# Kernel optimization log

Measured on AMD Instinct MI355X. Metric: run time of the kernel, lower is better.

Reference implementation:

```python
import jax, jax.numpy as jnp
import numpy as np

N_NODES = 50000
N_EDGES = 500000
IN_DIM = 64
OUT_DIM = 64
NUM_RELS = 16


def setup_inputs() -> dict:
    key = jax.random.key(0)
    ks = jax.random.split(key, 8)
    h = jax.random.normal(ks[0], (N_NODES, IN_DIM), dtype=jnp.float32)
    he = jax.random.normal(ks[1], (N_EDGES, IN_DIM), dtype=jnp.float32)
    src = jax.random.randint(ks[2], (N_EDGES,), 0, N_NODES)
    dst = jax.random.randint(ks[3], (N_EDGES,), 0, N_NODES)
    rel = jax.random.randint(ks[4], (N_EDGES,), 0, NUM_RELS)
    # xavier-ish scales
    W_shared = jax.random.normal(ks[5], (OUT_DIM, IN_DIM), dtype=jnp.float32) * (2.0 / (IN_DIM + OUT_DIM)) ** 0.5
    W_attn = jax.random.normal(ks[6], (1, 3 * OUT_DIM), dtype=jnp.float32) * (2.0 / (3 * OUT_DIM + 1)) ** 0.5
    W_rel = jax.random.normal(ks[7], (NUM_RELS, IN_DIM, OUT_DIM), dtype=jnp.float32) * (2.0 / (IN_DIM + OUT_DIM)) ** 0.5
    return {"h": h, "he": he, "src": src, "dst": dst, "rel": rel,
            "W_shared": W_shared, "W_attn": W_attn, "W_rel": W_rel}


def reference(h, he, src, dst, rel, W_shared, W_attn, W_rel):
    # --- edge attention: a = attn_fc([z_src, z_edge, z_dst]) (raw linear score, no softmax in original) ---
    Z = h @ W_shared.T                      # [N, out] project all nodes once
    ze = he @ W_shared.T                    # [E, out]
    # split attn weight to avoid materializing [E, 3*out] concat
    Wa_s, Wa_e, Wa_d = jnp.split(W_attn, 3, axis=1)   # each [1, out]
    a = Z[src] @ Wa_s.T + ze @ Wa_e.T + Z[dst] @ Wa_d.T   # [E, 1]
    # --- message: msg = (h_src @ W_rel[rel]) * a ---
    # compute per-(node, relation) transform once [N, R, out], then gather per edge
    H_all = jnp.einsum('ni,rio->nro', h, W_rel)          # [N, R, out]
    msg = H_all[src, rel] * a                             # [E, out]
    # --- scatter-sum aggregation into destination nodes ---
    out = jax.ops.segment_sum(msg, dst, num_segments=N_NODES)  # [N, out]
    # apply_func: activation (relu), no bias
    return jax.nn.relu(out)
```

## Files before the change

### kernel.cpp

```cpp
#include <hip/hip_runtime.h>
#include <math.h>

#define N_NODES 50000
#define N_EDGES 500000
#define DIM 64
#define NUM_RELS 16
#define GPB 64


__global__ void k0_prep(const float* __restrict__ W_shared,
                        const float* __restrict__ W_attn,
                        float* __restrict__ uvecs,
                        int* __restrict__ counts,
                        int* __restrict__ cursor) {
    int t = threadIdx.x;
    if (t < 64) {
        float us = 0.f, ve = 0.f, ud = 0.f;
        for (int o = 0; o < 64; ++o) {
            float w = W_shared[o * 64 + t];
            us = fmaf(w, W_attn[o],        us);
            ve = fmaf(w, W_attn[64 + o],   ve);
            ud = fmaf(w, W_attn[128 + o],  ud);
        }
        uvecs[t] = us; uvecs[64 + t] = ve; uvecs[128 + t] = ud;
    } else if (t < 80) {
        counts[t - 64] = 0;
    } else if (t < 96) {
        cursor[t - 80] = 0;
    }
}

__global__ void k1_node(const float* __restrict__ h,
                        const float* __restrict__ uvecs,
                        float* __restrict__ sn, float* __restrict__ dn,
                        float4* __restrict__ out4) {
    int n = blockIdx.x * blockDim.x + threadIdx.x;
    if (n >= N_NODES) return;
    const float* hp = h + (size_t)n * DIM;
    float s = 0.f, d = 0.f;
#pragma unroll
    for (int i = 0; i < 64; i += 4) {
        float4 t = *(const float4*)(hp + i);
        s = fmaf(t.x, uvecs[i],     s); s = fmaf(t.y, uvecs[i + 1], s);
        s = fmaf(t.z, uvecs[i + 2], s); s = fmaf(t.w, uvecs[i + 3], s);
        d = fmaf(t.x, uvecs[128 + i],     d); d = fmaf(t.y, uvecs[128 + i + 1], d);
        d = fmaf(t.z, uvecs[128 + i + 2], d); d = fmaf(t.w, uvecs[128 + i + 3], d);
    }
    sn[n] = s; dn[n] = d;
    float4 z = make_float4(0.f, 0.f, 0.f, 0.f);
#pragma unroll
    for (int i = 0; i < 16; ++i) out4[(size_t)n * 16 + i] = z;
}

__global__ void k2_ae(const float4* __restrict__ he4,
                      const int* __restrict__ src, const int* __restrict__ dst,
                      const int* __restrict__ rel,
                      const float* __restrict__ uvecs,
                      const float* __restrict__ sn, const float* __restrict__ dn,
                      float* __restrict__ ae, int* __restrict__ counts) {
    __shared__ int hist[NUM_RELS];
    int t = threadIdx.x;
    if (t < NUM_RELS) hist[t] = 0;
    __syncthreads();

    const int lane = t & 63;
    const int sub  = lane & 3;
    const int eo   = lane >> 2;
    const int gw   = blockIdx.x * 4 + (t >> 6);
    const int nw   = gridDim.x * 4;

    float4 u0 = *(const float4*)(uvecs + 64 + sub * 16 + 0);
    float4 u1 = *(const float4*)(uvecs + 64 + sub * 16 + 4);
    float4 u2 = *(const float4*)(uvecs + 64 + sub * 16 + 8);
    float4 u3 = *(const float4*)(uvecs + 64 + sub * 16 + 12);

    for (int base = gw * 16; base < N_EDGES; base += nw * 16) {
        int e = base + eo;
        float p = 0.f;
        if (e < N_EDGES) {
            const float4* row = he4 + (size_t)e * 16 + sub * 4;
            float4 a = row[0], b = row[1], c = row[2], d = row[3];
            p = a.x*u0.x + a.y*u0.y + a.z*u0.z + a.w*u0.w
              + b.x*u1.x + b.y*u1.y + b.z*u1.z + b.w*u1.w
              + c.x*u2.x + c.y*u2.y + c.z*u2.z + c.w*u2.w
              + d.x*u3.x + d.y*u3.y + d.z*u3.z + d.w*u3.w;
        }
        p += __shfl_xor(p, 1, 64);
        p += __shfl_xor(p, 2, 64);
        if (sub == 0 && e < N_EDGES) {
            ae[e] = p + sn[src[e]] + dn[dst[e]];
            atomicAdd(&hist[rel[e]], 1);
        }
    }
    __syncthreads();
    if (t < NUM_RELS && hist[t]) atomicAdd(&counts[t], hist[t]);
}

__global__ void k3_scan(const int* __restrict__ counts, int* __restrict__ offs) {
    int acc = 0;
    for (int r = 0; r < NUM_RELS; ++r) { offs[r] = acc; acc += counts[r]; }
    offs[NUM_RELS] = acc;
}

__global__ void k4_scatter(const int* __restrict__ rel,
                           const int* __restrict__ offs,
                           int* __restrict__ cursor,
                           int* __restrict__ perm) {
    __shared__ int hist[NUM_RELS];
    __shared__ int bbase[NUM_RELS];
    int t = threadIdx.x;
    if (t < NUM_RELS) hist[t] = 0;
    __syncthreads();
    int e = blockIdx.x * 1024 + t;
    int r = 0, lpos = 0;
    bool valid = (e < N_EDGES);
    if (valid) { r = rel[e]; lpos = atomicAdd(&hist[r], 1); }
    __syncthreads();
    if (t < NUM_RELS) bbase[t] = hist[t] ? atomicAdd(&cursor[t], hist[t]) : 0;
    __syncthreads();
    if (valid) perm[offs[r] + bbase[r] + lpos] = e;
}

__global__ __launch_bounds__(256, 4) void k5_main(
    const float* __restrict__ h,
    const int* __restrict__ src, const int* __restrict__ dst,
    const float* __restrict__ W_rel,
    const float* __restrict__ ae,
    const int* __restrict__ offs, const int* __restrict__ perm,
    float* __restrict__ out)
{
    const int lane = threadIdx.x & 63;
    const int wib  = __builtin_amdgcn_readfirstlane(threadIdx.x >> 6);
    const int r    = blockIdx.x & 15;
    const int g    = blockIdx.x >> 4;
    const int wr   = g * 4 + wib;
    const int WPR  = GPB * 4;

    float w[64];
    const float* wb = W_rel + (size_t)r * (DIM * DIM) + lane;
#pragma unroll
    for (int i = 0; i < 64; ++i) w[i] = wb[i * 64];
#pragma unroll
    for (int i = 0; i < 64; ++i) asm volatile("" : "+v"(w[i]));

    const int begin = offs[r];
    const int end   = offs[r + 1];

    for (int base = begin + wr * 64; base < end; base += WPR * 64) {
        int e_l = 0, s_l = 0, d_l = 0; float a_l = 0.f;
        if (base + lane < end) {
            e_l = perm[base + lane];
            s_l = src[e_l];
            d_l = dst[e_l];
            a_l = ae[e_l];
        }
        const int kmax = min(64, end - base);
        for (int k = 0; k < kmax; ++k) {
            const int   si = __builtin_amdgcn_readlane(s_l, k);
            const int   di = __builtin_amdgcn_readlane(d_l, k);
            const float ak = __int_as_float(__builtin_amdgcn_readlane(__float_as_int(a_l), k));

            const float* hp = h + (size_t)si * DIM;
            float a0 = 0.f, a1 = 0.f, a2 = 0.f, a3 = 0.f;
#pragma unroll
            for (int i = 0; i < 64; i += 4) {
                a0 = fmaf(hp[i],     w[i],     a0);
                a1 = fmaf(hp[i + 1], w[i + 1], a1);
                a2 = fmaf(hp[i + 2], w[i + 2], a2);
                a3 = fmaf(hp[i + 3], w[i + 3], a3);
            }
            const float dot = (a0 + a1) + (a2 + a3);
            unsafeAtomicAdd(out + (size_t)di * DIM + lane, ak * dot);
        }
    }
}

__global__ void k6_relu(float4* __restrict__ out, int n4) {
    int i = blockIdx.x * blockDim.x + threadIdx.x;
    if (i < n4) {
        float4 v = out[i];
        v.x = fmaxf(v.x, 0.f); v.y = fmaxf(v.y, 0.f);
        v.z = fmaxf(v.z, 0.f); v.w = fmaxf(v.w, 0.f);
        out[i] = v;
    }
}

extern "C" void kernel_launch(void* const* d_in, const int* in_sizes, int n_in,
                              void* d_out, int out_size, void* d_ws, size_t ws_size,
                              hipStream_t stream) {
    const float* h        = (const float*)d_in[0];
    const float* he       = (const float*)d_in[1];
    const int*   src      = (const int*)d_in[2];
    const int*   dst      = (const int*)d_in[3];
    const int*   rel      = (const int*)d_in[4];
    const float* W_shared = (const float*)d_in[5];
    const float* W_attn   = (const float*)d_in[6];
    const float* W_rel    = (const float*)d_in[7];
    float*       out      = (float*)d_out;

    float* uvecs  = (float*)d_ws;
    int*   counts = (int*)d_ws + 192;
    int*   offs   = (int*)d_ws + 208;
    int*   cursor = (int*)d_ws + 228;
    float* sn     = (float*)d_ws + 256;
    float* dn     = (float*)d_ws + 50256;
    float* ae     = (float*)d_ws + 100256;
    int*   perm   = (int*)d_ws + 600256;

    k0_prep<<<1, 128, 0, stream>>>(W_shared, W_attn, uvecs, counts, cursor);
    k1_node<<<(N_NODES + 255) / 256, 256, 0, stream>>>(h, uvecs, sn, dn, (float4*)out);
    k2_ae<<<1024, 256, 0, stream>>>((const float4*)he, src, dst, rel, uvecs, sn, dn, ae, counts);
    k3_scan<<<1, 1, 0, stream>>>(counts, offs);
    k4_scatter<<<(N_EDGES + 1023) / 1024, 1024, 0, stream>>>(rel, offs, cursor, perm);
    k5_main<<<NUM_RELS * GPB, 256, 0, stream>>>(h, src, dst, W_rel, ae, offs, perm, out);
    int n4 = out_size / 4;
    k6_relu<<<(n4 + 255) / 256, 256, 0, stream>>>((float4*)out, n4);
}
```

Measured before the change: 364.6 us.

## Fold prep and scan kernels into neighbors and unroll main edge loop by two

The attention-vector prep kernel is removed. Each block of the node and edge kernels now recomputes the projected attention vectors it needs into shared memory, and the node kernel also zeroes the counters. The single-thread scan kernel is also removed: scatter blocks and main blocks derive the relation offsets from the counts themselves. Two fewer launches and their serialization gaps are the aim, at the cost of some redundant per-block work. The main kernel handles two edges per iteration for more memory-level parallelism, and its grid grows from 64 to 160 groups per relation.

```diff
diff --git a/kernel.cpp b/kernel.cpp
--- a/kernel.cpp
+++ b/kernel.cpp
@@ -5,46 +5,41 @@
 #define N_EDGES 500000
 #define DIM 64
 #define NUM_RELS 16
-#define GPB 64
-
-
-__global__ void k0_prep(const float* __restrict__ W_shared,
+#define GPB 160
+
+
+__global__ void k1_node(const float* __restrict__ h,
+                        const float* __restrict__ W_shared,
                         const float* __restrict__ W_attn,
-                        float* __restrict__ uvecs,
-                        int* __restrict__ counts,
-                        int* __restrict__ cursor) {
+                        float* __restrict__ sn, float* __restrict__ dn,
+                        float4* __restrict__ out4,
+                        int* __restrict__ counts, int* __restrict__ cursor) {
+    __shared__ float sus[64], sud[64];
     int t = threadIdx.x;
     if (t < 64) {
-        float us = 0.f, ve = 0.f, ud = 0.f;
+        float us = 0.f, ud = 0.f;
         for (int o = 0; o < 64; ++o) {
             float w = W_shared[o * 64 + t];
-            us = fmaf(w, W_attn[o],        us);
-            ve = fmaf(w, W_attn[64 + o],   ve);
-            ud = fmaf(w, W_attn[128 + o],  ud);
-        }
-        uvecs[t] = us; uvecs[64 + t] = ve; uvecs[128 + t] = ud;
-    } else if (t < 80) {
-        counts[t - 64] = 0;
-    } else if (t < 96) {
-        cursor[t - 80] = 0;
-    }
-}
-
-__global__ void k1_node(const float* __restrict__ h,
-                        const float* __restrict__ uvecs,
-                        float* __restrict__ sn, float* __restrict__ dn,
-                        float4* __restrict__ out4) {
-    int n = blockIdx.x * blockDim.x + threadIdx.x;
+            us = fmaf(w, W_attn[o],       us);
+            ud = fmaf(w, W_attn[128 + o], ud);
+        }
+        sus[t] = us; sud[t] = ud;
+    }
+    if (t >= 64 && t < 80)  counts[t - 64] = 0;
+    if (t >= 80 && t < 96)  cursor[t - 80] = 0;
+    __syncthreads();
+
+    int n = blockIdx.x * blockDim.x + t;
     if (n >= N_NODES) return;
     const float* hp = h + (size_t)n * DIM;
     float s = 0.f, d = 0.f;
 #pragma unroll
     for (int i = 0; i < 64; i += 4) {
-        float4 t = *(const float4*)(hp + i);
-        s = fmaf(t.x, uvecs[i],     s); s = fmaf(t.y, uvecs[i + 1], s);
-        s = fmaf(t.z, uvecs[i + 2], s); s = fmaf(t.w, uvecs[i + 3], s);
-        d = fmaf(t.x, uvecs[128 + i],     d); d = fmaf(t.y, uvecs[128 + i + 1], d);
-        d = fmaf(t.z, uvecs[128 + i + 2], d); d = fmaf(t.w, uvecs[128 + i + 3], d);
+        float4 v = *(const float4*)(hp + i);
+        s = fmaf(v.x, sus[i], s);     s = fmaf(v.y, sus[i + 1], s);
+        s = fmaf(v.z, sus[i + 2], s); s = fmaf(v.w, sus[i + 3], s);
+        d = fmaf(v.x, sud[i], d);     d = fmaf(v.y, sud[i + 1], d);
+        d = fmaf(v.z, sud[i + 2], d); d = fmaf(v.w, sud[i + 3], d);
     }
     sn[n] = s; dn[n] = d;
     float4 z = make_float4(0.f, 0.f, 0.f, 0.f);
@@ -55,12 +50,20 @@
 __global__ void k2_ae(const float4* __restrict__ he4,
                       const int* __restrict__ src, const int* __restrict__ dst,
                       const int* __restrict__ rel,
-                      const float* __restrict__ uvecs,
+                      const float* __restrict__ W_shared,
+                      const float* __restrict__ W_attn,
                       const float* __restrict__ sn, const float* __restrict__ dn,
                       float* __restrict__ ae, int* __restrict__ counts) {
+    __shared__ float sve[64];
     __shared__ int hist[NUM_RELS];
     int t = threadIdx.x;
     if (t < NUM_RELS) hist[t] = 0;
+    if (t < 64) {
+        float ve = 0.f;
+        for (int o = 0; o < 64; ++o)
+            ve = fmaf(W_shared[o * 64 + t], W_attn[64 + o], ve);
+        sve[t] = ve;
+    }
     __syncthreads();
 
     const int lane = t & 63;
@@ -69,10 +72,10 @@
     const int gw   = blockIdx.x * 4 + (t >> 6);
     const int nw   = gridDim.x * 4;
 
-    float4 u0 = *(const float4*)(uvecs + 64 + sub * 16 + 0);
-    float4 u1 = *(const float4*)(uvecs + 64 + sub * 16 + 4);
-    float4 u2 = *(const float4*)(uvecs + 64 + sub * 16 + 8);
-    float4 u3 = *(const float4*)(uvecs + 64 + sub * 16 + 12);
+    float4 u0 = *(const float4*)(sve + sub * 16 + 0);
+    float4 u1 = *(const float4*)(sve + sub * 16 + 4);
+    float4 u2 = *(const float4*)(sve + sub * 16 + 8);
+    float4 u3 = *(const float4*)(sve + sub * 16 + 12);
 
     for (int base = gw * 16; base < N_EDGES; base += nw * 16) {
         int e = base + eo;
@@ -96,20 +99,19 @@
     if (t < NUM_RELS && hist[t]) atomicAdd(&counts[t], hist[t]);
 }
 
-__global__ void k3_scan(const int* __restrict__ counts, int* __restrict__ offs) {
-    int acc = 0;
-    for (int r = 0; r < NUM_RELS; ++r) { offs[r] = acc; acc += counts[r]; }
-    offs[NUM_RELS] = acc;
-}
-
 __global__ void k4_scatter(const int* __restrict__ rel,
-                           const int* __restrict__ offs,
+                           const int* __restrict__ counts,
                            int* __restrict__ cursor,
                            int* __restrict__ perm) {
     __shared__ int hist[NUM_RELS];
     __shared__ int bbase[NUM_RELS];
+    __shared__ int soffs[NUM_RELS];
     int t = threadIdx.x;
     if (t < NUM_RELS) hist[t] = 0;
+    if (t == 0) {
+        int acc = 0;
+        for (int j = 0; j < NUM_RELS; ++j) { soffs[j] = acc; acc += counts[j]; }
+    }
     __syncthreads();
     int e = blockIdx.x * 1024 + t;
     int r = 0, lpos = 0;
@@ -118,7 +120,7 @@
     __syncthreads();
     if (t < NUM_RELS) bbase[t] = hist[t] ? atomicAdd(&cursor[t], hist[t]) : 0;
     __syncthreads();
-    if (valid) perm[offs[r] + bbase[r] + lpos] = e;
+    if (valid) perm[soffs[r] + bbase[r] + lpos] = e;
 }
 
 __global__ __launch_bounds__(256, 4) void k5_main(
@@ -126,7 +128,7 @@
     const int* __restrict__ src, const int* __restrict__ dst,
     const float* __restrict__ W_rel,
     const float* __restrict__ ae,
-    const int* __restrict__ offs, const int* __restrict__ perm,
+    const int* __restrict__ counts, const int* __restrict__ perm,
     float* __restrict__ out)
 {
     const int lane = threadIdx.x & 63;
@@ -136,6 +138,15 @@
     const int wr   = g * 4 + wib;
     const int WPR  = GPB * 4;
 
+    int begin = 0, cr = 0;
+#pragma unroll
+    for (int j = 0; j < NUM_RELS; ++j) {
+        int c = counts[j];
+        if (j < r) begin += c;
+        if (j == r) cr = c;
+    }
+    const int end = begin + cr;
+
     float w[64];
     const float* wb = W_rel + (size_t)r * (DIM * DIM) + lane;
 #pragma unroll
@@ -143,34 +154,48 @@
 #pragma unroll
     for (int i = 0; i < 64; ++i) asm volatile("" : "+v"(w[i]));
 
-    const int begin = offs[r];
-    const int end   = offs[r + 1];
-
     for (int base = begin + wr * 64; base < end; base += WPR * 64) {
-        int e_l = 0, s_l = 0, d_l = 0; float a_l = 0.f;
+        int s_l = 0, d_l = 0; float a_l = 0.f;
         if (base + lane < end) {
-            e_l = perm[base + lane];
+            int e_l = perm[base + lane];
             s_l = src[e_l];
             d_l = dst[e_l];
             a_l = ae[e_l];
         }
         const int kmax = min(64, end - base);
-        for (int k = 0; k < kmax; ++k) {
-            const int   si = __builtin_amdgcn_readlane(s_l, k);
-            const int   di = __builtin_amdgcn_readlane(d_l, k);
+        int k = 0;
+        for (; k + 2 <= kmax; k += 2) {
+            const int si0 = __builtin_amdgcn_readlane(s_l, k);
+            const int si1 = __builtin_amdgcn_readlane(s_l, k + 1);
+            const int di0 = __builtin_amdgcn_readlane(d_l, k);
+            const int di1 = __builtin_amdgcn_readlane(d_l, k + 1);
+            const float a0 = __int_as_float(__builtin_amdgcn_readlane(__float_as_int(a_l), k));
+            const float a1 = __int_as_float(__builtin_amdgcn_readlane(__float_as_int(a_l), k + 1));
+            const float* hp0 = h + (size_t)si0 * DIM;
+            const float* hp1 = h + (size_t)si1 * DIM;
+            float x0 = 0.f, y0 = 0.f, x1 = 0.f, y1 = 0.f;
+#pragma unroll
+            for (int i = 0; i < 64; i += 2) {
+                x0 = fmaf(hp0[i],     w[i],     x0);
+                x1 = fmaf(hp1[i],     w[i],     x1);
+                y0 = fmaf(hp0[i + 1], w[i + 1], y0);
+                y1 = fmaf(hp1[i + 1], w[i + 1], y1);
+            }
+            unsafeAtomicAdd(out + (size_t)di0 * DIM + lane, a0 * (x0 + y0));
+            unsafeAtomicAdd(out + (size_t)di1 * DIM + lane, a1 * (x1 + y1));
+        }
+        if (k < kmax) {
+            const int si = __builtin_amdgcn_readlane(s_l, k);
+            const int di = __builtin_amdgcn_readlane(d_l, k);
             const float ak = __int_as_float(__builtin_amdgcn_readlane(__float_as_int(a_l), k));
-
             const float* hp = h + (size_t)si * DIM;
-            float a0 = 0.f, a1 = 0.f, a2 = 0.f, a3 = 0.f;
-#pragma unroll
-            for (int i = 0; i < 64; i += 4) {
-                a0 = fmaf(hp[i],     w[i],     a0);
-                a1 = fmaf(hp[i + 1], w[i + 1], a1);
-                a2 = fmaf(hp[i + 2], w[i + 2], a2);
-                a3 = fmaf(hp[i + 3], w[i + 3], a3);
+            float x = 0.f, y = 0.f;
+#pragma unroll
+            for (int i = 0; i < 64; i += 2) {
+                x = fmaf(hp[i],     w[i],     x);
+                y = fmaf(hp[i + 1], w[i + 1], y);
             }
-            const float dot = (a0 + a1) + (a2 + a3);
-            unsafeAtomicAdd(out + (size_t)di * DIM + lane, ak * dot);
+            unsafeAtomicAdd(out + (size_t)di * DIM + lane, ak * (x + y));
         }
     }
 }
@@ -198,21 +223,19 @@
     const float* W_rel    = (const float*)d_in[7];
     float*       out      = (float*)d_out;
 
-    float* uvecs  = (float*)d_ws;
     int*   counts = (int*)d_ws + 192;
-    int*   offs   = (int*)d_ws + 208;
     int*   cursor = (int*)d_ws + 228;
     float* sn     = (float*)d_ws + 256;
     float* dn     = (float*)d_ws + 50256;
     float* ae     = (float*)d_ws + 100256;
     int*   perm   = (int*)d_ws + 600256;
 
-    k0_prep<<<1, 128, 0, stream>>>(W_shared, W_attn, uvecs, counts, cursor);
-    k1_node<<<(N_NODES + 255) / 256, 256, 0, stream>>>(h, uvecs, sn, dn, (float4*)out);
-    k2_ae<<<1024, 256, 0, stream>>>((const float4*)he, src, dst, rel, uvecs, sn, dn, ae, counts);
-    k3_scan<<<1, 1, 0, stream>>>(counts, offs);
-    k4_scatter<<<(N_EDGES + 1023) / 1024, 1024, 0, stream>>>(rel, offs, cursor, perm);
-    k5_main<<<NUM_RELS * GPB, 256, 0, stream>>>(h, src, dst, W_rel, ae, offs, perm, out);
+    k1_node<<<(N_NODES + 255) / 256, 256, 0, stream>>>(h, W_shared, W_attn, sn, dn,
+                                                       (float4*)out, counts, cursor);
+    k2_ae<<<1024, 256, 0, stream>>>((const float4*)he, src, dst, rel, W_shared, W_attn,
+                                    sn, dn, ae, counts);
+    k4_scatter<<<(N_EDGES + 1023) / 1024, 1024, 0, stream>>>(rel, counts, cursor, perm);
+    k5_main<<<NUM_RELS * GPB, 256, 0, stream>>>(h, src, dst, W_rel, ae, counts, perm, out);
     int n4 = out_size / 4;
     k6_relu<<<(n4 + 255) / 256, 256, 0, stream>>>((float4*)out, n4);
 }
```

Result: slower. 382.7 us (+5.0%).
